# Kernel optimization log

Hardware: AMD Instinct MI355X
Metric: run time of the kernel (lower is better)

Reference implementation:

```python
import jax, jax.numpy as jnp
import numpy as np

N_NODES = 100000
N_EDGES = 1600000
D_IN = 128
D_HID = 16
N_CLASSES = 40


def _glorot(key, shape):
    lim = float(np.sqrt(6.0 / (shape[0] + shape[1])))
    return jax.random.uniform(key, shape, jnp.float32, -lim, lim)


def setup_inputs() -> dict:
    key = jax.random.key(0)
    ks = jax.random.split(key, 8)
    x = jax.random.normal(ks[0], (N_NODES, D_IN), dtype=jnp.float32)
    edge_index = jax.random.randint(ks[1], (2, N_EDGES), 0, N_NODES, dtype=jnp.int64)
    return {
        "x": x,
        "edge_index": edge_index,
        # conv1: SAGEConv(D_IN, D_HID): lin_l (on aggregated, with bias), lin_r (on root, no bias)
        "W1l": _glorot(ks[2], (D_IN, D_HID)),
        "b1": jnp.zeros((D_HID,), jnp.float32),
        "W1r": _glorot(ks[3], (D_IN, D_HID)),
        # conv2: SAGEConv(D_HID, N_CLASSES)
        "W2l": _glorot(ks[4], (D_HID, N_CLASSES)),
        "b2": jnp.zeros((N_CLASSES,), jnp.float32),
        "W2r": _glorot(ks[5], (D_HID, N_CLASSES)),
    }


def _sage_conv(x, src, dst, Wl, bl, Wr, num_nodes):
    # mean aggregation of source-node features into destination nodes
    summed = jax.ops.segment_sum(x[src], dst, num_segments=num_nodes)  # [N, D]
    cnt = jax.ops.segment_sum(jnp.ones_like(dst, dtype=x.dtype), dst, num_segments=num_nodes)
    agg = summed / jnp.maximum(cnt, 1.0)[:, None]
    return agg @ Wl + bl + x @ Wr


def reference(x, edge_index, W1l, b1, W1r, W2l, b2, W2r):
    src, dst = edge_index[0], edge_index[1]
    n = x.shape[0]
    h = jax.nn.relu(_sage_conv(x, src, dst, W1l, b1, W1r, n))
    # F.dropout with training=self.training; module evaluated in eval mode -> identity
    out = _sage_conv(h, src, dst, W2l, b2, W2r, n)
    return jax.nn.log_softmax(out, axis=1)
```

## Files before the change

### kernel.cpp

```cpp
#include <hip/hip_runtime.h>
#include <math.h>

typedef _Float16 f16;

constexpr int NN   = 100000;
constexpr int DIN  = 128;
constexpr int DH   = 16;
constexpr int NC   = 40;
constexpr int CAP  = 48;
constexpr int NBKT = (NN + 255) / 256;
constexpr int BCAP = 6144;

static_assert(NN % 32 == 0 || NN % 8 == 0, "agg grids assume NN % 8 == 0");

template <bool VEC4>
__global__ void k_part(const int* __restrict__ src, const int* __restrict__ dst, int E,
                       int* __restrict__ bcur, int* __restrict__ part)
{
    __shared__ int lh[NBKT];
    __shared__ int lbase[NBKT];
    int t = threadIdx.x;
    for (int i = t; i < NBKT; i += 1024) lh[i] = 0;
    __syncthreads();
    long base = (long)blockIdx.x * 8192;
    int pk[8], bk[8], rk[8];
    if (VEC4 && base + 8192 <= (long)E) {
        const int4* s4 = (const int4*)(src + base) + t * 2;
        const int4* d4 = (const int4*)(dst + base) + t * 2;
        int4 sa = s4[0], sb = s4[1];
        int4 da = d4[0], db = d4[1];
        int ss[8] = {sa.x, sa.y, sa.z, sa.w, sb.x, sb.y, sb.z, sb.w};
        int dd[8] = {da.x, da.y, da.z, da.w, db.x, db.y, db.z, db.w};
        #pragma unroll
        for (int i = 0; i < 8; ++i) {
            bk[i] = dd[i] >> 8;
            pk[i] = (ss[i] << 8) | (dd[i] & 255);
            rk[i] = atomicAdd(&lh[bk[i]], 1);
        }
    } else {
        #pragma unroll
        for (int i = 0; i < 8; ++i) {
            long e = base + (long)t * 8 + i;
            if (e < E) {
                int s = src[e], d = dst[e];
                bk[i] = d >> 8;
                pk[i] = (s << 8) | (d & 255);
                rk[i] = atomicAdd(&lh[bk[i]], 1);
            } else bk[i] = -1;
        }
    }
    __syncthreads();
    for (int i = t; i < NBKT; i += 1024)
        lbase[i] = lh[i] ? atomicAdd(&bcur[i], lh[i]) : 0;
    __syncthreads();
    #pragma unroll
    for (int i = 0; i < 8; ++i) {
        if (bk[i] >= 0) {
            int idx = lbase[bk[i]] + rk[i];
            if (idx < BCAP) part[(long)bk[i] * BCAP + idx] = pk[i];
        }
    }
}

__global__ void k_pb(const int* __restrict__ bcur, const int* __restrict__ part,
                     int* __restrict__ cnt, int* __restrict__ col,
                     const float* __restrict__ x,
                     const float* __restrict__ W1l, const float* __restrict__ W1r,
                     f16* __restrict__ p1h, float* __restrict__ p1r)
{
    __shared__ int   cur[256];
    __shared__ float ps[2][64][DH + 1];
    int t = threadIdx.x;
    if ((int)blockIdx.x < NBKT) {
        int b = blockIdx.x;
        cur[t] = 0;
        __syncthreads();
        long base = (long)b * BCAP;
        int n = min(bcur[b], BCAP);
        for (int e = t; e < n; e += 256) {
            int pk = part[base + e];
            int dl = pk & 255;
            int r  = atomicAdd(&cur[dl], 1);
            if (r < CAP) col[((long)((b << 8) + dl)) * CAP + r] = pk >> 8;
        }
        __syncthreads();
        int node = (b << 8) + t;
        if (node < NN) cnt[node] = cur[t];
        return;
    }
    int nl = t & 63;
    int halfu = __builtin_amdgcn_readfirstlane((t >> 6) & 1);
    int khu   = __builtin_amdgcn_readfirstlane(t >> 7);
    long n  = (long)((int)blockIdx.x - NBKT) * 64 + nl;
    long ncl = n < NN ? n : NN - 1;
    const float4* xr = (const float4*)(x + ncl * DIN + khu * 64);
    const float*  Wk = (halfu ? W1r : W1l) + khu * 64 * DH;

    float acc[DH];
    #pragma unroll
    for (int j = 0; j < DH; ++j) acc[j] = 0.f;
    #pragma unroll
    for (int k4 = 0; k4 < 16; ++k4) {
        float4 v = xr[k4];
        const float* wr = Wk + k4 * 4 * DH;
        #pragma unroll
        for (int j = 0; j < DH; ++j) {
            acc[j] = fmaf(v.x, wr[j],          acc[j]);
            acc[j] = fmaf(v.y, wr[DH + j],     acc[j]);
            acc[j] = fmaf(v.z, wr[2 * DH + j], acc[j]);
            acc[j] = fmaf(v.w, wr[3 * DH + j], acc[j]);
        }
    }
    if (khu) {
        #pragma unroll
        for (int j = 0; j < DH; ++j) ps[halfu][nl][j] = acc[j];
    }
    __syncthreads();
    if (!khu && n < NN) {
        #pragma unroll
        for (int j = 0; j < DH; ++j) acc[j] += ps[halfu][nl][j];
        if (halfu == 0) {
            union { f16 f[16]; uint4 q[2]; } u;
            #pragma unroll
            for (int j = 0; j < DH; ++j) u.f[j] = (f16)acc[j];
            uint4* po = (uint4*)(p1h + n * DH);
            po[0] = u.q[0]; po[1] = u.q[1];
        } else {
            float4* pr = (float4*)(p1r + n * DH);
            pr[0] = make_float4(acc[0],  acc[1],  acc[2],  acc[3]);
            pr[1] = make_float4(acc[4],  acc[5],  acc[6],  acc[7]);
            pr[2] = make_float4(acc[8],  acc[9],  acc[10], acc[11]);
            pr[3] = make_float4(acc[12], acc[13], acc[14], acc[15]);
        }
    }
}

__global__ void k_agg1(const int* __restrict__ cnt, const int* __restrict__ col,
                       const uint4* __restrict__ g4, const float4* __restrict__ p1r4,
                       const float* __restrict__ b1, uint4* __restrict__ h4)
{
    int t    = threadIdx.x;
    int lane = t & 63;
    int wv   = (blockIdx.x * blockDim.x + t) >> 6;
    int n    = wv * 8 + (lane >> 3);
    int dh   = (lane >> 2) & 1;
    int ng   = lane & 3;
    int degf = (n < NN) ? cnt[n] : 0;
    int deg  = min(degf, CAP);
    const int* cb = col + (long)n * CAP;
    float a[8];
    #pragma unroll
    for (int j = 0; j < 8; ++j) a[j] = 0.f;
    int i = ng;
    for (; i + 12 < deg; i += 16) {
        int s0 = cb[i], s1 = cb[i+4], s2 = cb[i+8], s3 = cb[i+12];
        uint4 v0 = g4[(long)s0*2+dh], v1 = g4[(long)s1*2+dh],
              v2 = g4[(long)s2*2+dh], v3 = g4[(long)s3*2+dh];
        const f16 *p0=(const f16*)&v0, *p1=(const f16*)&v1,
                  *p2=(const f16*)&v2, *p3=(const f16*)&v3;
        #pragma unroll
        for (int j = 0; j < 8; ++j)
            a[j] += (float)p0[j] + (float)p1[j] + (float)p2[j] + (float)p3[j];
    }
    for (; i < deg; i += 4) {
        int s = cb[i];
        uint4 v = g4[(long)s*2+dh];
        const f16* p = (const f16*)&v;
        #pragma unroll
        for (int j = 0; j < 8; ++j) a[j] += (float)p[j];
    }
    #pragma unroll
    for (int j = 0; j < 8; ++j) {
        a[j] += __shfl_xor(a[j], 1);
        a[j] += __shfl_xor(a[j], 2);
    }
    if (ng == 0 && n < NN) {
        float inv = 1.0f / fmaxf((float)degf, 1.0f);
        float4 bl = ((const float4*)b1)[dh*2+0];
        float4 bh = ((const float4*)b1)[dh*2+1];
        float4 rl = p1r4[(long)n*4 + dh*2+0];
        float4 rh = p1r4[(long)n*4 + dh*2+1];
        float bb[8] = {bl.x,bl.y,bl.z,bl.w, bh.x,bh.y,bh.z,bh.w};
        float rr[8] = {rl.x,rl.y,rl.z,rl.w, rh.x,rh.y,rh.z,rh.w};
        union { f16 f[8]; uint4 u; } o;
        #pragma unroll
        for (int j = 0; j < 8; ++j)
            o.f[j] = (f16)fmaxf(fmaf(a[j], inv, bb[j] + rr[j]), 0.f);
        h4[(long)n*2+dh] = o.u;
    }
}

__global__ void k_agg2o(const int* __restrict__ cnt, const int* __restrict__ col,
                        const uint4* __restrict__ g4,
                        const float* __restrict__ W2l, const float* __restrict__ b2,
                        const float* __restrict__ W2r, float* __restrict__ out)
{
    __shared__ float sW[2 * DH * NC + NC];
    __shared__ float sA[32][DH + 1];
    __shared__ float sH[32][DH + 1];
    int t = threadIdx.x;
    for (int i = t; i < DH * NC; i += 256) {
        sW[i]           = W2l[i];
        sW[DH * NC + i] = W2r[i];
    }
    if (t < NC) sW[2 * DH * NC + t] = b2[t];

    int lane = t & 63;
    int wv   = (blockIdx.x * 256 + t) >> 6;
    int n    = wv * 8 + (lane >> 3);
    int dh   = (lane >> 2) & 1;
    int ng   = lane & 3;
    int nl2  = t >> 3;
    int degf = cnt[n];
    int deg  = min(degf, CAP);
    const int* cb = col + (long)n * CAP;
    float a[8];
    #pragma unroll
    for (int j = 0; j < 8; ++j) a[j] = 0.f;
    int i = ng;
    for (; i + 12 < deg; i += 16) {
        int s0 = cb[i], s1 = cb[i+4], s2 = cb[i+8], s3 = cb[i+12];
        uint4 v0 = g4[(long)s0*2+dh], v1 = g4[(long)s1*2+dh],
              v2 = g4[(long)s2*2+dh], v3 = g4[(long)s3*2+dh];
        const f16 *p0=(const f16*)&v0, *p1=(const f16*)&v1,
                  *p2=(const f16*)&v2, *p3=(const f16*)&v3;
        #pragma unroll
        for (int j = 0; j < 8; ++j)
            a[j] += (float)p0[j] + (float)p1[j] + (float)p2[j] + (float)p3[j];
    }
    for (; i < deg; i += 4) {
        int s = cb[i];
        uint4 v = g4[(long)s*2+dh];
        const f16* p = (const f16*)&v;
        #pragma unroll
        for (int j = 0; j < 8; ++j) a[j] += (float)p[j];
    }
    #pragma unroll
    for (int j = 0; j < 8; ++j) {
        a[j] += __shfl_xor(a[j], 1);
        a[j] += __shfl_xor(a[j], 2);
    }
    if (ng == 0) {
        float inv = 1.0f / fmaxf((float)degf, 1.0f);
        #pragma unroll
        for (int j = 0; j < 8; ++j) sA[nl2][dh*8+j] = a[j] * inv;
    } else if (ng == 1) {
        uint4 hv4 = g4[(long)n*2+dh];
        const f16* hp = (const f16*)&hv4;
        #pragma unroll
        for (int j = 0; j < 8; ++j) sH[nl2][dh*8+j] = (float)hp[j];
    }
    __syncthreads();

    float av[DH], hv[DH];
    #pragma unroll
    for (int j = 0; j < DH; ++j) { av[j] = sA[nl2][j]; hv[j] = sH[nl2][j]; }
    int lane8 = t & 7;
    float o[5];
    #pragma unroll
    for (int j = 0; j < 5; ++j) {
        int c = lane8 + 8 * j;
        float acc = sW[2 * DH * NC + c];
        #pragma unroll
        for (int k = 0; k < DH; ++k) {
            acc = fmaf(av[k], sW[k * NC + c],           acc);
            acc = fmaf(hv[k], sW[DH * NC + k * NC + c], acc);
        }
        o[j] = acc;
    }
    float mx = o[0];
    #pragma unroll
    for (int j = 1; j < 5; ++j) mx = fmaxf(mx, o[j]);
    #pragma unroll
    for (int m = 1; m <= 4; m <<= 1) mx = fmaxf(mx, __shfl_xor(mx, m));
    float s = 0.f;
    #pragma unroll
    for (int j = 0; j < 5; ++j) s += __expf(o[j] - mx);
    #pragma unroll
    for (int m = 1; m <= 4; m <<= 1) s += __shfl_xor(s, m);
    float lg = mx + __logf(s);
    float* op = out + (long)n * NC;
    #pragma unroll
    for (int j = 0; j < 5; ++j) op[lane8 + 8 * j] = o[j] - lg;
}


extern "C" void kernel_launch(void* const* d_in, const int* in_sizes, int n_in,
                              void* d_out, int out_size, void* d_ws, size_t ws_size,
                              hipStream_t stream) {
    const float* x   = (const float*)d_in[0];
    const int*   ei  = (const int*)d_in[1];
    const float* W1l = (const float*)d_in[2];
    const float* b1  = (const float*)d_in[3];
    const float* W1r = (const float*)d_in[4];
    const float* W2l = (const float*)d_in[5];
    const float* b2  = (const float*)d_in[6];
    const float* W2r = (const float*)d_in[7];
    float* out = (float*)d_out;

    const int E = in_sizes[1] / 2;
    const int* src = ei;
    const int* dst = ei + E;

    int* bcur = (int*)d_ws;
    int* cnt  = bcur + 512;
    int* col  = cnt + NN;
    int* part = col + (long)NN * CAP;
    float* p1r = (float*)(part + (long)NBKT * BCAP);
    f16*   p1h = (f16*)(p1r + (long)NN * DH);
    f16*   h   = p1h + (long)NN * DH;

    hipMemsetAsync(bcur, 0, NBKT * sizeof(int), stream);

    if ((E & 3) == 0)
        k_part<true ><<<(E + 8191) / 8192, 1024, 0, stream>>>(src, dst, E, bcur, part);
    else
        k_part<false><<<(E + 8191) / 8192, 1024, 0, stream>>>(src, dst, E, bcur, part);

    const int PB = (NN + 63) / 64;
    k_pb<<<NBKT + PB, 256, 0, stream>>>(bcur, part, cnt, col, x, W1l, W1r, p1h, p1r);

    k_agg1 <<<(NN + 31) / 32, 256, 0, stream>>>(cnt, col, (const uint4*)p1h,
                                                (const float4*)p1r, b1, (uint4*)h);
    k_agg2o<<<(NN + 31) / 32, 256, 0, stream>>>(cnt, col, (const uint4*)h,
                                                W2l, b2, W2r, out);
}
```

Baseline: 196.7 us.

## Fuse edge partitioning with layer-1 projection and bucket CSR build with aggregation

Moves the layer-1 dense projection into the edge-partition launch as extra blocks, so the partition and matmul work run in one grid. The per-bucket CSR build is merged with the first aggregation: neighbor lists are built in shared memory, written out for layer 2, and consumed directly from LDS. Buckets shrink from 256 to 128 nodes, and the global bucket counters are padded to separate cache lines to reduce atomic contention. This removes one launch and a global round-trip of the column array for layer 1. In exchange it uses a large LDS footprint per block and has fewer, bigger aggregation blocks, and the projection no longer splits K across waves.

```diff
diff --git a/kernel.cpp b/kernel.cpp
--- a/kernel.cpp
+++ b/kernel.cpp
@@ -8,101 +8,80 @@
 constexpr int DH   = 16;
 constexpr int NC   = 40;
 constexpr int CAP  = 48;
-constexpr int NBKT = (NN + 255) / 256;
-constexpr int BCAP = 6144;
-
-static_assert(NN % 32 == 0 || NN % 8 == 0, "agg grids assume NN % 8 == 0");
+constexpr int NB   = (NN + 127) / 128;
+constexpr int BC   = 2816;
+constexpr int BSTR = 16;
+
+static_assert(NN % 8 == 0, "agg grids assume NN % 8 == 0");
 
 template <bool VEC4>
-__global__ void k_part(const int* __restrict__ src, const int* __restrict__ dst, int E,
-                       int* __restrict__ bcur, int* __restrict__ part)
+__global__ __launch_bounds__(1024)
+void k_pp(const int* __restrict__ src, const int* __restrict__ dst, int E, int PBp,
+          int* __restrict__ bcur, int* __restrict__ part,
+          const float* __restrict__ x,
+          const float* __restrict__ W1l, const float* __restrict__ W1r,
+          f16* __restrict__ p1h, float* __restrict__ p1r)
 {
-    __shared__ int lh[NBKT];
-    __shared__ int lbase[NBKT];
+    __shared__ int lh[NB];
+    __shared__ int lbase[NB];
     int t = threadIdx.x;
-    for (int i = t; i < NBKT; i += 1024) lh[i] = 0;
-    __syncthreads();
-    long base = (long)blockIdx.x * 8192;
-    int pk[8], bk[8], rk[8];
-    if (VEC4 && base + 8192 <= (long)E) {
-        const int4* s4 = (const int4*)(src + base) + t * 2;
-        const int4* d4 = (const int4*)(dst + base) + t * 2;
-        int4 sa = s4[0], sb = s4[1];
-        int4 da = d4[0], db = d4[1];
-        int ss[8] = {sa.x, sa.y, sa.z, sa.w, sb.x, sb.y, sb.z, sb.w};
-        int dd[8] = {da.x, da.y, da.z, da.w, db.x, db.y, db.z, db.w};
-        #pragma unroll
-        for (int i = 0; i < 8; ++i) {
-            bk[i] = dd[i] >> 8;
-            pk[i] = (ss[i] << 8) | (dd[i] & 255);
-            rk[i] = atomicAdd(&lh[bk[i]], 1);
-        }
-    } else {
-        #pragma unroll
-        for (int i = 0; i < 8; ++i) {
-            long e = base + (long)t * 8 + i;
-            if (e < E) {
-                int s = src[e], d = dst[e];
-                bk[i] = d >> 8;
-                pk[i] = (s << 8) | (d & 255);
+    if ((int)blockIdx.x < PBp) {
+        for (int i = t; i < NB; i += 1024) lh[i] = 0;
+        __syncthreads();
+        long base = (long)blockIdx.x * 8192;
+        int pk[8], bk[8], rk[8];
+        if (VEC4 && base + 8192 <= (long)E) {
+            const int4* s4 = (const int4*)(src + base) + t * 2;
+            const int4* d4 = (const int4*)(dst + base) + t * 2;
+            int4 sa = s4[0], sb = s4[1];
+            int4 da = d4[0], db = d4[1];
+            int ss[8] = {sa.x, sa.y, sa.z, sa.w, sb.x, sb.y, sb.z, sb.w};
+            int dd[8] = {da.x, da.y, da.z, da.w, db.x, db.y, db.z, db.w};
+            #pragma unroll
+            for (int i = 0; i < 8; ++i) {
+                bk[i] = dd[i] >> 7;
+                pk[i] = (ss[i] << 7) | (dd[i] & 127);
                 rk[i] = atomicAdd(&lh[bk[i]], 1);
-            } else bk[i] = -1;
-        }
-    }
-    __syncthreads();
-    for (int i = t; i < NBKT; i += 1024)
-        lbase[i] = lh[i] ? atomicAdd(&bcur[i], lh[i]) : 0;
-    __syncthreads();
-    #pragma unroll
-    for (int i = 0; i < 8; ++i) {
-        if (bk[i] >= 0) {
-            int idx = lbase[bk[i]] + rk[i];
-            if (idx < BCAP) part[(long)bk[i] * BCAP + idx] = pk[i];
-        }
-    }
-}
-
-__global__ void k_pb(const int* __restrict__ bcur, const int* __restrict__ part,
-                     int* __restrict__ cnt, int* __restrict__ col,
-                     const float* __restrict__ x,
-                     const float* __restrict__ W1l, const float* __restrict__ W1r,
-                     f16* __restrict__ p1h, float* __restrict__ p1r)
-{
-    __shared__ int   cur[256];
-    __shared__ float ps[2][64][DH + 1];
-    int t = threadIdx.x;
-    if ((int)blockIdx.x < NBKT) {
-        int b = blockIdx.x;
-        cur[t] = 0;
-        __syncthreads();
-        long base = (long)b * BCAP;
-        int n = min(bcur[b], BCAP);
-        for (int e = t; e < n; e += 256) {
-            int pk = part[base + e];
-            int dl = pk & 255;
-            int r  = atomicAdd(&cur[dl], 1);
-            if (r < CAP) col[((long)((b << 8) + dl)) * CAP + r] = pk >> 8;
+            }
+        } else {
+            #pragma unroll
+            for (int i = 0; i < 8; ++i) {
+                long e = base + (long)t * 8 + i;
+                if (e < E) {
+                    int s = src[e], d = dst[e];
+                    bk[i] = d >> 7;
+                    pk[i] = (s << 7) | (d & 127);
+                    rk[i] = atomicAdd(&lh[bk[i]], 1);
+                } else bk[i] = -1;
+            }
         }
         __syncthreads();
-        int node = (b << 8) + t;
-        if (node < NN) cnt[node] = cur[t];
+        for (int i = t; i < NB; i += 1024)
+            lbase[i] = lh[i] ? atomicAdd(&bcur[i * BSTR], lh[i]) : 0;
+        __syncthreads();
+        #pragma unroll
+        for (int i = 0; i < 8; ++i) {
+            if (bk[i] >= 0) {
+                int idx = lbase[bk[i]] + rk[i];
+                if (idx < BC) part[(long)bk[i] * BC + idx] = pk[i];
+            }
+        }
         return;
     }
-    int nl = t & 63;
-    int halfu = __builtin_amdgcn_readfirstlane((t >> 6) & 1);
-    int khu   = __builtin_amdgcn_readfirstlane(t >> 7);
-    long n  = (long)((int)blockIdx.x - NBKT) * 64 + nl;
-    long ncl = n < NN ? n : NN - 1;
-    const float4* xr = (const float4*)(x + ncl * DIN + khu * 64);
-    const float*  Wk = (halfu ? W1r : W1l) + khu * 64 * DH;
-
+    int bp = (int)blockIdx.x - PBp;
+    int w  = t >> 6;
+    int halfu = __builtin_amdgcn_readfirstlane(w & 1);
+    long n = (long)bp * 512 + ((long)(w >> 1) << 6) + (t & 63);
+    if (n >= NN) return;
+    const float4* xr = (const float4*)(x + n * DIN);
+    const float*  W  = halfu ? W1r : W1l;
     float acc[DH];
     #pragma unroll
     for (int j = 0; j < DH; ++j) acc[j] = 0.f;
-    #pragma unroll
-    for (int k4 = 0; k4 < 16; ++k4) {
+    #pragma unroll 8
+    for (int k4 = 0; k4 < 32; ++k4) {
         float4 v = xr[k4];
-        const float* wr = Wk + k4 * 4 * DH;
+        const float* wr = W + k4 * 4 * DH;
         #pragma unroll
         for (int j = 0; j < DH; ++j) {
             acc[j] = fmaf(v.x, wr[j],          acc[j]);
@@ -111,49 +90,59 @@
             acc[j] = fmaf(v.w, wr[3 * DH + j], acc[j]);
         }
     }
-    if (khu) {
-        #pragma unroll
-        for (int j = 0; j < DH; ++j) ps[halfu][nl][j] = acc[j];
-    }
+    if (halfu == 0) {
+        union { f16 f[16]; uint4 q[2]; } u;
+        #pragma unroll
+        for (int j = 0; j < DH; ++j) u.f[j] = (f16)acc[j];
+        uint4* po = (uint4*)(p1h + n * DH);
+        po[0] = u.q[0]; po[1] = u.q[1];
+    } else {
+        float4* pr = (float4*)(p1r + n * DH);
+        pr[0] = make_float4(acc[0],  acc[1],  acc[2],  acc[3]);
+        pr[1] = make_float4(acc[4],  acc[5],  acc[6],  acc[7]);
+        pr[2] = make_float4(acc[8],  acc[9],  acc[10], acc[11]);
+        pr[3] = make_float4(acc[12], acc[13], acc[14], acc[15]);
+    }
+}
+
+__global__ __launch_bounds__(512)
+void k_ba1(const int* __restrict__ bcur, const int* __restrict__ part,
+           const uint4* __restrict__ g4, const float4* __restrict__ p1r4,
+           const float* __restrict__ b1,
+           int* __restrict__ cnt, int* __restrict__ col, uint4* __restrict__ h4)
+{
+    __shared__ int scol[128 * CAP];
+    __shared__ int cur[128];
+    int t = threadIdx.x, b = blockIdx.x;
+    if (t < 128) cur[t] = 0;
     __syncthreads();
-    if (!khu && n < NN) {
-        #pragma unroll
-        for (int j = 0; j < DH; ++j) acc[j] += ps[halfu][nl][j];
-        if (halfu == 0) {
-            union { f16 f[16]; uint4 q[2]; } u;
-            #pragma unroll
-            for (int j = 0; j < DH; ++j) u.f[j] = (f16)acc[j];
-            uint4* po = (uint4*)(p1h + n * DH);
-            po[0] = u.q[0]; po[1] = u.q[1];
-        } else {
-            float4* pr = (float4*)(p1r + n * DH);
-            pr[0] = make_float4(acc[0],  acc[1],  acc[2],  acc[3]);
-            pr[1] = make_float4(acc[4],  acc[5],  acc[6],  acc[7]);
-            pr[2] = make_float4(acc[8],  acc[9],  acc[10], acc[11]);
-            pr[3] = make_float4(acc[12], acc[13], acc[14], acc[15]);
-        }
-    }
-}
-
-__global__ void k_agg1(const int* __restrict__ cnt, const int* __restrict__ col,
-                       const uint4* __restrict__ g4, const float4* __restrict__ p1r4,
-                       const float* __restrict__ b1, uint4* __restrict__ h4)
-{
-    int t    = threadIdx.x;
-    int lane = t & 63;
-    int wv   = (blockIdx.x * blockDim.x + t) >> 6;
-    int n    = wv * 8 + (lane >> 3);
-    int dh   = (lane >> 2) & 1;
-    int ng   = lane & 3;
-    int degf = (n < NN) ? cnt[n] : 0;
+    long base = (long)b * BC;
+    int ne = min(bcur[b * BSTR], BC);
+    for (int e = t; e < ne; e += 512) {
+        int pk = part[base + e];
+        int dl = pk & 127;
+        int r  = atomicAdd(&cur[dl], 1);
+        if (r < CAP) scol[dl * CAP + r] = pk >> 7;
+    }
+    __syncthreads();
+    if (t < 128) {
+        int node = (b << 7) + t;
+        if (node < NN) cnt[node] = cur[t];
+    }
+    int* gcol = col + (long)b * 128 * CAP;
+    for (int i = t; i < 128 * CAP; i += 512) gcol[i] = scol[i];
+
+    int nl = t >> 2, dh = (t >> 1) & 1, ng = t & 1;
+    int node = (b << 7) + nl;
+    int degf = cur[nl];
     int deg  = min(degf, CAP);
-    const int* cb = col + (long)n * CAP;
+    const int* cb = scol + nl * CAP;
     float a[8];
     #pragma unroll
     for (int j = 0; j < 8; ++j) a[j] = 0.f;
     int i = ng;
-    for (; i + 12 < deg; i += 16) {
-        int s0 = cb[i], s1 = cb[i+4], s2 = cb[i+8], s3 = cb[i+12];
+    for (; i + 6 < deg; i += 8) {
+        int s0 = cb[i], s1 = cb[i+2], s2 = cb[i+4], s3 = cb[i+6];
         uint4 v0 = g4[(long)s0*2+dh], v1 = g4[(long)s1*2+dh],
               v2 = g4[(long)s2*2+dh], v3 = g4[(long)s3*2+dh];
         const f16 *p0=(const f16*)&v0, *p1=(const f16*)&v1,
@@ -162,7 +151,7 @@
         for (int j = 0; j < 8; ++j)
             a[j] += (float)p0[j] + (float)p1[j] + (float)p2[j] + (float)p3[j];
     }
-    for (; i < deg; i += 4) {
+    for (; i < deg; i += 2) {
         int s = cb[i];
         uint4 v = g4[(long)s*2+dh];
         const f16* p = (const f16*)&v;
@@ -170,23 +159,20 @@
         for (int j = 0; j < 8; ++j) a[j] += (float)p[j];
     }
     #pragma unroll
-    for (int j = 0; j < 8; ++j) {
-        a[j] += __shfl_xor(a[j], 1);
-        a[j] += __shfl_xor(a[j], 2);
-    }
-    if (ng == 0 && n < NN) {
+    for (int j = 0; j < 8; ++j) a[j] += __shfl_xor(a[j], 1);
+    if (ng == 0 && node < NN) {
         float inv = 1.0f / fmaxf((float)degf, 1.0f);
         float4 bl = ((const float4*)b1)[dh*2+0];
         float4 bh = ((const float4*)b1)[dh*2+1];
-        float4 rl = p1r4[(long)n*4 + dh*2+0];
-        float4 rh = p1r4[(long)n*4 + dh*2+1];
+        float4 rl = p1r4[(long)node*4 + dh*2+0];
+        float4 rh = p1r4[(long)node*4 + dh*2+1];
         float bb[8] = {bl.x,bl.y,bl.z,bl.w, bh.x,bh.y,bh.z,bh.w};
         float rr[8] = {rl.x,rl.y,rl.z,rl.w, rh.x,rh.y,rh.z,rh.w};
         union { f16 f[8]; uint4 u; } o;
         #pragma unroll
         for (int j = 0; j < 8; ++j)
             o.f[j] = (f16)fmaxf(fmaf(a[j], inv, bb[j] + rr[j]), 0.f);
-        h4[(long)n*2+dh] = o.u;
+        h4[(long)node*2+dh] = o.u;
     }
 }
 
@@ -303,25 +289,26 @@
     const int* dst = ei + E;
 
     int* bcur = (int*)d_ws;
-    int* cnt  = bcur + 512;
+    int* cnt  = bcur + 12544;
     int* col  = cnt + NN;
-    int* part = col + (long)NN * CAP;
-    float* p1r = (float*)(part + (long)NBKT * BCAP);
+    int* part = col + (long)NB * 128 * CAP;
+    float* p1r = (float*)(part + (long)NB * BC);
     f16*   p1h = (f16*)(p1r + (long)NN * DH);
     f16*   h   = p1h + (long)NN * DH;
 
-    hipMemsetAsync(bcur, 0, NBKT * sizeof(int), stream);
-
+    hipMemsetAsync(bcur, 0, NB * BSTR * sizeof(int), stream);
+
+    const int PBp = (E + 8191) / 8192;
+    const int PBj = (NN + 511) / 512;
     if ((E & 3) == 0)
-        k_part<true ><<<(E + 8191) / 8192, 1024, 0, stream>>>(src, dst, E, bcur, part);
+        k_pp<true ><<<PBp + PBj, 1024, 0, stream>>>(src, dst, E, PBp, bcur, part,
+                                                    x, W1l, W1r, p1h, p1r);
     else
-        k_part<false><<<(E + 8191) / 8192, 1024, 0, stream>>>(src, dst, E, bcur, part);
-
-    const int PB = (NN + 63) / 64;
-    k_pb<<<NBKT + PB, 256, 0, stream>>>(bcur, part, cnt, col, x, W1l, W1r, p1h, p1r);
-
-    k_agg1 <<<(NN + 31) / 32, 256, 0, stream>>>(cnt, col, (const uint4*)p1h,
-                                                (const float4*)p1r, b1, (uint4*)h);
+        k_pp<false><<<PBp + PBj, 1024, 0, stream>>>(src, dst, E, PBp, bcur, part,
+                                                    x, W1l, W1r, p1h, p1r);
+
+    k_ba1  <<<NB, 512, 0, stream>>>(bcur, part, (const uint4*)p1h,
+                                    (const float4*)p1r, b1, cnt, col, (uint4*)h);
     k_agg2o<<<(NN + 31) / 32, 256, 0, stream>>>(cnt, col, (const uint4*)h,
                                                 W2l, b2, W2r, out);
 }
```

Result: faster. 182.7 us (-7.1%).
